# Kernel tuning notes

Measured on AMD Instinct MI355X. Metric: run time of the kernel, lower is better.

Reference implementation:

```python
import jax, jax.numpy as jnp
import numpy as np

B, L, H, NH, HD, M, NL, V, RD, NS = 4, 512, 768, 12, 64, 3072, 6, 32000, 128, 2
EPS = 1e-12
COEF = 1.0 / float(np.sqrt(HD))
NEG_INF = float('-inf')


def _ln(x, scale, bias):
    x = x - jnp.mean(x, axis=-1, keepdims=True)
    x = x * jax.lax.rsqrt(jnp.mean(jnp.square(x), axis=-1, keepdims=True) + EPS)
    return x * scale + bias


def setup_inputs() -> dict:
    key = jax.random.key(0)
    ks = jax.random.split(key, 16)
    def p(k, shape):
        return jax.random.normal(k, shape, jnp.float32) * 0.02
    return dict(
        token_ids=jax.random.randint(ks[0], (B, L), 0, V, jnp.int32),
        segment_ids=jax.random.randint(ks[1], (B, L), 0, NS, jnp.int32),
        input_mask=jnp.ones((B, L), jnp.int32),
        tok_emb=p(ks[2], (V, H)),
        seg_emb=p(ks[3], (NS, H)),
        emb_scale=jnp.ones((H,), jnp.float32),
        emb_bias=jnp.zeros((H,), jnp.float32),
        Wq=p(ks[4], (NL, H, NH, HD)), bq=jnp.zeros((NL, NH, HD), jnp.float32),
        Wk=p(ks[5], (NL, H, NH, HD)), bk=jnp.zeros((NL, NH, HD), jnp.float32),
        Wv=p(ks[6], (NL, H, NH, HD)), bv=jnp.zeros((NL, NH, HD), jnp.float32),
        relpos=p(ks[7], (NL, 2 * RD - 1, H)),
        Wo=p(ks[8], (NL, NH, HD, H)), bo=jnp.zeros((NL, H), jnp.float32),
        ln1_s=jnp.ones((NL, H), jnp.float32), ln1_b=jnp.zeros((NL, H), jnp.float32),
        W1=p(ks[9], (NL, H, M)), b1=jnp.zeros((NL, M), jnp.float32),
        W2=p(ks[10], (NL, M, H)), b2=jnp.zeros((NL, H), jnp.float32),
        ln2_s=jnp.ones((NL, H), jnp.float32), ln2_b=jnp.zeros((NL, H), jnp.float32),
    )


def _encoder(token_ids, segment_ids, input_mask,
             tok_emb, seg_emb, emb_scale, emb_bias,
             Wq, bq, Wk, bk, Wv, bv, relpos, Wo, bo,
             ln1_s, ln1_b, W1, b1, W2, b2, ln2_s, ln2_b):
    # Embedding block: token + segment embeddings, layer norm (dropout = eval/no-op)
    x = tok_emb[token_ids] + seg_emb[segment_ids]            # [B, L, H]
    x = _ln(x, emb_scale, emb_bias)
    mask = jnp.where(input_mask.astype(bool), 0.0, NEG_INF)[:, None, None, :]  # [B,1,1,L]

    for i in range(NL):
        # --- relative-position self-attention ---
        q = jnp.einsum('bqe,ehd->bqhd', x, Wq[i]) + bq[i]
        k = jnp.einsum('bke,ehd->bkhd', x, Wk[i]) + bk[i]
        v = jnp.einsum('bke,ehd->bkhd', x, Wv[i]) + bv[i]
        att = jnp.einsum('bqhd,bkhd->bhqk', q, k) + mask      # [B,NH,L,L]
        # skew trick: embed absolute [L,L] scores into relative [L, 2L-1] layout
        att = jnp.pad(att, [(0, 0), (0, 0), (0, 0), (0, L - 2)], constant_values=NEG_INF)
        att = att.reshape(att.shape[:2] + (L * (2 * L - 2),))
        att = jnp.pad(att, [(0, 0), (0, 0), (L - 1, 1)], constant_values=NEG_INF)
        att = att.reshape(att.shape[:2] + (L, 2 * L - 1))     # [B,NH,L,2L-1]
        # relative-position key/value embeddings, edge-padded to 2L-1 rows
        pad = L - RD
        rel_emb = jnp.pad(relpos[i], [(pad, pad), (0, 0)], mode='edge')  # [2L-1, H]
        k_rel = jnp.einsum('re,ehd->rhd', rel_emb, Wk[i]) + bk[i]
        att = (att + jnp.einsum('bqhd,rhd->bhqr', q, k_rel)) * COEF
        probs = jax.nn.softmax(att, axis=-1)                  # [B,NH,L,2L-1]
        v_rel = jnp.einsum('re,ehd->rhd', rel_emb, Wv[i]) + bv[i]
        rel_ctx = jnp.einsum('bhqr,rhd->bqhd', probs, v_rel)
        # un-skew probs back to [B,NH,L,L] for the absolute-position context
        p = probs.reshape(probs.shape[:2] + (L * (2 * L - 1),))[:, :, L - 1:-1]
        p = p.reshape(probs.shape[:2] + (L, 2 * L - 2))[:, :, :, :L]
        ctx = jnp.einsum('bhqk,bkhd->bqhd', p, v) + rel_ctx
        y = jnp.einsum('bqhd,hde->bqe', ctx, Wo[i]) + bo[i]
        x = _ln(x + y, ln1_s[i], ln1_b[i])
        # --- MLP block ---
        y = jax.nn.gelu(jnp.einsum('bqe,em->bqm', x, W1[i]) + b1[i])
        y = jnp.einsum('bqm,me->bqe', y, W2[i]) + b2[i]
        x = _ln(x + y, ln2_s[i], ln2_b[i])
    return x


def reference(token_ids, segment_ids, input_mask,
              tok_emb, seg_emb, emb_scale, emb_bias,
              Wq, bq, Wk, bk, Wv, bv, relpos, Wo, bo,
              ln1_s, ln1_b, W1, b1, W2, b2, ln2_s, ln2_b):
    return _encoder(token_ids, segment_ids, input_mask,
                    tok_emb, seg_emb, emb_scale, emb_bias,
                    Wq, bq, Wk, bk, Wv, bv, relpos, Wo, bo,
                    ln1_s, ln1_b, W1, b1, W2, b2, ln2_s, ln2_b)
```

## Files before the change

kernel.cpp:

```cpp
#include <hip/hip_runtime.h>
#include <hip/hip_bf16.h>
#include <math.h>

#define B_   4
#define L_   512
#define H_   768
#define NH_  12
#define HD_  64
#define M_   3072
#define NL_  6
#define RD_  128
#define NR_  255
#define ROWS (B_*L_)
#define MEXT 2304
#define COEF_ 0.125f

typedef __attribute__((ext_vector_type(8))) short bf16x8;
typedef __attribute__((ext_vector_type(4))) float f32x4;


static __device__ __forceinline__ float wave_reduce_sum(float v) {
#pragma unroll
    for (int off = 32; off > 0; off >>= 1) v += __shfl_xor(v, off, 64);
    return v;
}

static __device__ __forceinline__ float gelu_f(float x) {
    float x3 = x * x * x;
    return 0.5f * x * (1.f + tanhf(0.7978845608028654f * (x + 0.044715f * x3)));
}

static __device__ __forceinline__ unsigned short f2bfu(float v) {
    __hip_bfloat16 h = __float2bfloat16(v);
    return *(unsigned short*)&h;
}

static __device__ __forceinline__ float bfu2f(unsigned short u) {
    union { float f; unsigned int i; } x;
    x.i = ((unsigned int)u) << 16;
    return x.f;
}

static __device__ __forceinline__ void gload16(const void* g, void* l) {
    __builtin_amdgcn_global_load_lds(
        (const __attribute__((address_space(1))) void*)g,
        (__attribute__((address_space(3))) void*)l,
        16, 0, 0);
}


__global__ __launch_bounds__(256) void embed_ln_kernel(
    const int* __restrict__ tok, const int* __restrict__ seg,
    const float* __restrict__ temb, const float* __restrict__ semb,
    const float* __restrict__ sc, const float* __restrict__ bi,
    float* __restrict__ out, __hip_bfloat16* __restrict__ outb)
{
    int row = blockIdx.x;
    int t = threadIdx.x;
    int tid = tok[row], sid = seg[row];
    const float* tp = temb + (size_t)tid * H_;
    const float* sp = semb + (size_t)sid * H_;
    float v[3];
#pragma unroll
    for (int j = 0; j < 3; j++) { int idx = t + j * 256; v[j] = tp[idx] + sp[idx]; }

    __shared__ float red[4];
    __shared__ float bc;
    int lane = t & 63, wid = t >> 6;

    float s = v[0] + v[1] + v[2];
    s = wave_reduce_sum(s);
    if (lane == 0) red[wid] = s;
    __syncthreads();
    if (t == 0) bc = (red[0] + red[1] + red[2] + red[3]) * (1.f / H_);
    __syncthreads();
    float mean = bc;

    float c[3]; float ss = 0.f;
#pragma unroll
    for (int j = 0; j < 3; j++) { c[j] = v[j] - mean; ss += c[j] * c[j]; }
    ss = wave_reduce_sum(ss);
    __syncthreads();
    if (lane == 0) red[wid] = ss;
    __syncthreads();
    if (t == 0) bc = rsqrtf((red[0] + red[1] + red[2] + red[3]) * (1.f / H_) + 1e-12f);
    __syncthreads();
    float r = bc;
#pragma unroll
    for (int j = 0; j < 3; j++) {
        int idx = t + j * 256;
        float o = c[j] * r * sc[idx] + bi[idx];
        out[(size_t)row * H_ + idx] = o;
        outb[(size_t)row * H_ + idx] = __float2bfloat16(o);
    }
}


__global__ __launch_bounds__(256) void add_ln_kernel(
    const float* __restrict__ x, const float* __restrict__ p0,
    const float* __restrict__ p1, const float* __restrict__ p2,
    const float* __restrict__ bias,
    const float* __restrict__ sc, const float* __restrict__ bi,
    float* __restrict__ out, __hip_bfloat16* __restrict__ outb)
{
    int row = blockIdx.x;
    int t = threadIdx.x;
    const float* xp = x + (size_t)row * H_;
    const float* q0 = p0 + (size_t)row * H_;
    const float* q1 = p1 ? p1 + (size_t)row * H_ : nullptr;
    const float* q2 = p2 ? p2 + (size_t)row * H_ : nullptr;
    float v[3];
#pragma unroll
    for (int j = 0; j < 3; j++) {
        int idx = t + j * 256;
        float a = xp[idx] + q0[idx];
        if (q1) a += q1[idx];
        if (q2) a += q2[idx];
        if (bias) a += bias[idx];
        v[j] = a;
    }

    __shared__ float red[4];
    __shared__ float bc;
    int lane = t & 63, wid = t >> 6;

    float s = v[0] + v[1] + v[2];
    s = wave_reduce_sum(s);
    if (lane == 0) red[wid] = s;
    __syncthreads();
    if (t == 0) bc = (red[0] + red[1] + red[2] + red[3]) * (1.f / H_);
    __syncthreads();
    float mean = bc;

    float c[3]; float ss = 0.f;
#pragma unroll
    for (int j = 0; j < 3; j++) { c[j] = v[j] - mean; ss += c[j] * c[j]; }
    ss = wave_reduce_sum(ss);
    __syncthreads();
    if (lane == 0) red[wid] = ss;
    __syncthreads();
    if (t == 0) bc = rsqrtf((red[0] + red[1] + red[2] + red[3]) * (1.f / H_) + 1e-12f);
    __syncthreads();
    float r = bc;
#pragma unroll
    for (int j = 0; j < 3; j++) {
        int idx = t + j * 256;
        float o = c[j] * r * sc[idx] + bi[idx];
        out[(size_t)row * H_ + idx] = o;
        if (outb) outb[(size_t)row * H_ + idx] = __float2bfloat16(o);
    }
}


__global__ __launch_bounds__(256) void pack_all_kernel(
    const float* __restrict__ Wq, const float* __restrict__ Wk, const float* __restrict__ Wv,
    const float* __restrict__ Wo, const float* __restrict__ W1, const float* __restrict__ W2,
    const float* __restrict__ bq, const float* __restrict__ bk, const float* __restrict__ bv,
    const float* __restrict__ relpos,
    __hip_bfloat16* __restrict__ WtQ6, __hip_bfloat16* __restrict__ WtO6,
    __hip_bfloat16* __restrict__ WtW16, __hip_bfloat16* __restrict__ WtW26,
    float* __restrict__ qkvbias6, __hip_bfloat16* __restrict__ relb6)
{
    const int l = blockIdx.z / 7;
    const int zz = blockIdx.z % 7;
    const int t = threadIdx.x;
    if (zz == 6) {
        int id = blockIdx.y * 48 + blockIdx.x;
        if (id < 192) {
            int i = id * 1024 + t * 4;
            if (i < NR_ * H_) {
                float4 v = *(const float4*)(relpos + (size_t)l * NR_ * H_ + i);
                ushort4 o;
                o.x = f2bfu(v.x); o.y = f2bfu(v.y); o.z = f2bfu(v.z); o.w = f2bfu(v.w);
                *(ushort4*)((unsigned short*)relb6 + (size_t)l * NR_ * H_ + i) = o;
            }
        } else if (id < 201) {
            int i = (id - 192) * 256 + t;
            if (i < 2304) {
                float v = i < 768 ? bq[(size_t)l * H_ + i]
                        : (i < 1536 ? bk[(size_t)l * H_ + i - 768]
                                    : bv[(size_t)l * H_ + i - 1536]);
                qkvbias6[(size_t)l * 2304 + i] = v;
            }
        }
        return;
    }
    const float* in; __hip_bfloat16* out; int K, N;
    int bx = blockIdx.x, by = blockIdx.y;
    if (zz < 4) {
        if (bx >= 12) return;
        K = 768; N = 768;
        in = (zz == 0) ? Wq + (size_t)l * H_ * H_
           : (zz == 1) ? Wk + (size_t)l * H_ * H_
           : (zz == 2) ? Wv + (size_t)l * H_ * H_
                       : Wo + (size_t)l * H_ * H_;
        out = (zz < 3) ? WtQ6 + (size_t)l * 3 * H_ * H_ + (size_t)zz * H_ * H_
                       : WtO6 + (size_t)l * H_ * H_;
    } else if (zz == 4) {
        K = 768; N = 3072;
        in = W1 + (size_t)l * H_ * M_; out = WtW16 + (size_t)l * M_ * H_;
    } else {
        K = 3072; N = 768;
        in = W2 + (size_t)l * M_ * H_; out = WtW26 + (size_t)l * H_ * M_;
        int tmp = bx; bx = by; by = tmp;
    }
    __shared__ float tile[64][68];
    const int bX = bx * 64;
    const int bY = by * 64;
    {
        int r = t >> 2, c0 = (t & 3) * 16;
        const float* src = in + (size_t)(bY + r) * N + bX + c0;
#pragma unroll
        for (int i = 0; i < 4; i++)
            *(float4*)&tile[r][c0 + i * 4] = *(const float4*)(src + i * 4);
    }
    __syncthreads();
    {
        int n = t >> 2, k0 = (t & 3) * 16;
        unsigned short ov[16];
#pragma unroll
        for (int i = 0; i < 16; i++) ov[i] = f2bfu(tile[k0 + i][n]);
        unsigned short* dst = (unsigned short*)out + (size_t)(bX + n) * K + bY + k0;
        *(uint4*)dst       = *(uint4*)&ov[0];
        *(uint4*)(dst + 8) = *(uint4*)&ov[8];
    }
}


__global__ __launch_bounds__(256) void transpose_vvr_kernel(
    const __hip_bfloat16* __restrict__ qkvb,
    __hip_bfloat16* __restrict__ vT, __hip_bfloat16* __restrict__ vrT)
{
    __shared__ unsigned short tile[64][72];
    const int bx = blockIdx.x;
    const int h  = blockIdx.y;
    const int t = threadIdx.x;
    const int r = t >> 2, c0 = (t & 3) * 16;
    if (bx < 32) {
        const int kb = bx * 64;
        const unsigned short* src = (const unsigned short*)qkvb + (size_t)(kb + r) * 2304 + 1536 + h * 64 + c0;
        *(uint4*)&tile[r][c0]     = *(const uint4*)src;
        *(uint4*)&tile[r][c0 + 8] = *(const uint4*)(src + 8);
        __syncthreads();
        unsigned short outv[16];
#pragma unroll
        for (int i = 0; i < 16; i++) outv[i] = tile[c0 + i][r];
        unsigned short* dst = (unsigned short*)vT +
            ((size_t)((kb >> 9) * NH_ + h) * 64 + r) * 512 + (kb & 511) + c0;
        *(uint4*)dst       = *(uint4*)&outv[0];
        *(uint4*)(dst + 8) = *(uint4*)&outv[8];
    } else {
        const int jb = (bx - 32) * 64;
        const int j = jb + r;
        if (j < NR_) {
            const unsigned short* src = (const unsigned short*)qkvb + (size_t)(2048 + j) * 2304 + 1536 + h * 64 + c0;
            *(uint4*)&tile[r][c0]     = *(const uint4*)src;
            *(uint4*)&tile[r][c0 + 8] = *(const uint4*)(src + 8);
        } else {
#pragma unroll
            for (int i = 0; i < 16; i++) tile[r][c0 + i] = 0;
        }
        __syncthreads();
        unsigned short outv[16];
#pragma unroll
        for (int i = 0; i < 16; i++) outv[i] = tile[c0 + i][r];
        unsigned short* dst = (unsigned short*)vrT + ((size_t)(h * 64) + r) * 256 + jb + c0;
        *(uint4*)dst       = *(uint4*)&outv[0];
        *(uint4*)(dst + 8) = *(uint4*)&outv[8];
    }
}


#define TK 64

__global__ __launch_bounds__(512, 6) void gemm_bf16_kernel(
    const __hip_bfloat16* __restrict__ A, const __hip_bfloat16* __restrict__ A2,
    const __hip_bfloat16* __restrict__ Bt,
    const float* __restrict__ bias, float* __restrict__ Cf, __hip_bfloat16* __restrict__ Cb,
    float* __restrict__ CfX, size_t xstride,
    int M, int N, int K, int act, int ksplit)
{
    __shared__ __hip_bfloat16 As[2][128 * TK];
    __shared__ __hip_bfloat16 Bs[2][64 * TK];
    const int t = threadIdx.x;
    const int lane = t & 63;
    const int wid = t >> 6;
    const int lq = lane & 15, lg = lane >> 4;
    const int wm = (wid & 3) * 32, wn = (wid >> 2) * 32;

    const int nbx = gridDim.x;
    const int nwg = nbx * gridDim.y;
    int wgid = blockIdx.y * nbx + blockIdx.x;
    if ((nwg & 7) == 0) { int qq = nwg >> 3; wgid = (wgid & 7) * qq + (wgid >> 3); }
    const int bm = (wgid / nbx) * 128, bn = (wgid % nbx) * 64;
    const int kbase = blockIdx.z * ksplit;

    f32x4 acc[2][2];
#pragma unroll
    for (int i = 0; i < 2; i++)
#pragma unroll
        for (int j = 0; j < 2; j++) acc[i][j] = (f32x4){0.f, 0.f, 0.f, 0.f};

    const int rl = t >> 3;
    const int cswz = (((t & 7) * 16) ^ ((rl & 7) << 4)) >> 1;
    const __hip_bfloat16* ga[2];
    const __hip_bfloat16* gb;
    int lofsA[2], lofsB;
#pragma unroll
    for (int c = 0; c < 2; c++) {
        int rowa = bm + c * 64 + rl;
        const __hip_bfloat16* base;
        if (A2 && rowa >= ROWS) {
            int rr = rowa - ROWS; if (rr > NR_ - 1) rr = NR_ - 1;
            base = A2 + (size_t)rr * K;
        } else {
            if (rowa >= M) rowa = M - 1;
            base = A + (size_t)rowa * K;
        }
        ga[c] = base + kbase + cswz;
        lofsA[c] = (c * 64 + wid * 8) * TK;
    }
    gb = Bt + (size_t)(bn + rl) * K + kbase + cswz;
    lofsB = (wid * 8) * TK;

    const int nt = ksplit / TK;
    gload16(ga[0], &As[0][lofsA[0]]);
    gload16(ga[1], &As[0][lofsA[1]]);
    gload16(gb,    &Bs[0][lofsB]);
    __syncthreads();

    int cur = 0;
    for (int kt = 0; kt < nt; kt++) {
        if (kt + 1 < nt) {
            const int koff = (kt + 1) * TK;
            gload16(ga[0] + koff, &As[cur ^ 1][lofsA[0]]);
            gload16(ga[1] + koff, &As[cur ^ 1][lofsA[1]]);
            gload16(gb + koff,    &Bs[cur ^ 1][lofsB]);
        }
#pragma unroll
        for (int kh = 0; kh < 2; kh++) {
            const int kb = kh * 64 + lg * 16;
            bf16x8 af[2], bfr[2];
#pragma unroll
            for (int i = 0; i < 2; i++) {
                int ra = wm + i * 16 + lq;
                af[i] = *(const bf16x8*)((const char*)&As[cur][0] + ra * 128 + (kb ^ ((ra & 7) << 4)));
            }
#pragma unroll
            for (int j = 0; j < 2; j++) {
                int rb = wn + j * 16 + lq;
                bfr[j] = *(const bf16x8*)((const char*)&Bs[cur][0] + rb * 128 + (kb ^ ((rb & 7) << 4)));
            }
#pragma unroll
            for (int i = 0; i < 2; i++)
#pragma unroll
                for (int j = 0; j < 2; j++)
                    acc[i][j] = __builtin_amdgcn_mfma_f32_16x16x32_bf16(af[i], bfr[j], acc[i][j], 0, 0, 0);
        }
        __syncthreads();
        cur ^= 1;
    }

    float* outf = (blockIdx.z == 0) ? Cf : (CfX + (size_t)(blockIdx.z - 1) * xstride);
#pragma unroll
    for (int i = 0; i < 2; i++) {
#pragma unroll
        for (int j = 0; j < 2; j++) {
            int col = bn + wn + j * 16 + lq;
            float bsv = bias ? bias[col] : 0.f;
            int row0 = bm + wm + i * 16 + lg * 4;
#pragma unroll
            for (int rr = 0; rr < 4; rr++) {
                int row = row0 + rr;
                if (row >= M) continue;
                float v = acc[i][j][rr] + bsv;
                if (act) v = gelu_f(v);
                if (Cb && blockIdx.z == 0) Cb[(size_t)row * N + col] = __float2bfloat16(v);
                else                       outf[(size_t)row * N + col] = v;
            }
        }
    }
}


#define PS_LD 520
#define PR_LD 264

__global__ __launch_bounds__(256, 3) void attn_kernel(
    const __hip_bfloat16* __restrict__ qkvb,
    const __hip_bfloat16* __restrict__ vT,
    const __hip_bfloat16* __restrict__ vrT,
    const int* __restrict__ mask,
    __hip_bfloat16* __restrict__ ctxb)
{
    __shared__ unsigned short RqPrel[32 * PR_LD];
    __shared__ unsigned short Ps[32 * PS_LD];
    __shared__ float mstat[32 * 4];
    __shared__ float sstat[32 * 4];
    __shared__ float maskb[512];

    const int i_ = blockIdx.x;
    const int c_ = i_ & 7, s_ = i_ >> 3;
    const int p_ = c_ + 8 * (s_ >> 4);
    const int qt = s_ & 15;
    const int b = p_ / 12, h = p_ % 12;

    const int t = threadIdx.x;
    const int lane = t & 63, w = t >> 6;
    const int lq = lane & 15, lg = lane >> 4;

    maskb[t]       = mask[b * L_ + t]       ? 0.f : -1e30f;
    maskb[t + 256] = mask[b * L_ + t + 256] ? 0.f : -1e30f;

    const char* Qbase  = (const char*)qkvb + ((size_t)(b * L_ + qt * 32) * 2304 + h * 64) * 2;
    const char* Kbase  = (const char*)qkvb + ((size_t)(b * L_) * 2304 + 768 + h * 64) * 2;
    const char* KRbase = (const char*)qkvb + ((size_t)2048 * 2304 + 768 + h * 64) * 2;

    bf16x8 afq[2][2];
#pragma unroll
    for (int ks = 0; ks < 2; ks++) {
        const int kofs = ks * 64 + lg * 16;
        afq[ks][0] = *(const bf16x8*)(Qbase + (size_t)lq * 4608 + kofs);
        afq[ks][1] = *(const bf16x8*)(Qbase + (size_t)(16 + lq) * 4608 + kofs);
    }

    f32x4 accr[2][4];
#pragma unroll
    for (int i = 0; i < 2; i++)
#pragma unroll
        for (int j = 0; j < 4; j++) accr[i][j] = (f32x4){0.f, 0.f, 0.f, 0.f};
#pragma unroll
    for (int ks = 0; ks < 2; ks++) {
        const int kofs = ks * 64 + lg * 16;
        bf16x8 bkr_[4];
#pragma unroll
        for (int jt = 0; jt < 4; jt++) {
            int j = w * 64 + jt * 16 + lq;
            int jr = j > 254 ? 254 : j;
            bkr_[jt] = *(const bf16x8*)(KRbase + (size_t)jr * 4608 + kofs);
        }
#pragma unroll
        for (int jt = 0; jt < 4; jt++) {
            accr[0][jt] = __builtin_amdgcn_mfma_f32_16x16x32_bf16(afq[ks][0], bkr_[jt], accr[0][jt], 0, 0, 0);
            accr[1][jt] = __builtin_amdgcn_mfma_f32_16x16x32_bf16(afq[ks][1], bkr_[jt], accr[1][jt], 0, 0, 0);
        }
    }

    bf16x8 bk0_[8], bk1_[8];
#pragma unroll
    for (int jt = 0; jt < 8; jt++) {
        int key = w * 128 + jt * 16 + lq;
        bk0_[jt] = *(const bf16x8*)(Kbase + (size_t)key * 4608 + lg * 16);
        bk1_[jt] = *(const bf16x8*)(Kbase + (size_t)key * 4608 + 64 + lg * 16);
    }

#pragma unroll
    for (int it = 0; it < 2; it++)
#pragma unroll
        for (int jt = 0; jt < 4; jt++)
#pragma unroll
            for (int r = 0; r < 4; r++)
                RqPrel[(it * 16 + lg * 4 + r) * PR_LD + w * 64 + jt * 16 + lq] = f2bfu(accr[it][jt][r]);

    f32x4 accs[2][8];
#pragma unroll
    for (int i = 0; i < 2; i++)
#pragma unroll
        for (int j = 0; j < 8; j++) accs[i][j] = (f32x4){0.f, 0.f, 0.f, 0.f};
#pragma unroll
    for (int jt = 0; jt < 8; jt++) {
        accs[0][jt] = __builtin_amdgcn_mfma_f32_16x16x32_bf16(afq[0][0], bk0_[jt], accs[0][jt], 0, 0, 0);
        accs[1][jt] = __builtin_amdgcn_mfma_f32_16x16x32_bf16(afq[0][1], bk0_[jt], accs[1][jt], 0, 0, 0);
    }
#pragma unroll
    for (int jt = 0; jt < 8; jt++) {
        accs[0][jt] = __builtin_amdgcn_mfma_f32_16x16x32_bf16(afq[1][0], bk1_[jt], accs[0][jt], 0, 0, 0);
        accs[1][jt] = __builtin_amdgcn_mfma_f32_16x16x32_bf16(afq[1][1], bk1_[jt], accs[1][jt], 0, 0, 0);
    }

    const __hip_bfloat16* vTb  = vT  + (((size_t)(b * NH_ + h) * 64) + w * 16 + lq) * 512 + lg * 8;
    const __hip_bfloat16* vrTb = vrT + ((size_t)(h * 64) + w * 16 + lq) * 256 + lg * 8;
    bf16x8 vrpre[8];
#pragma unroll
    for (int ks = 0; ks < 8; ks++)
        vrpre[ks] = *(const bf16x8*)(vrTb + ks * 32);

    __syncthreads();

#pragma unroll
    for (int it = 0; it < 2; it++) {
#pragma unroll
        for (int r = 0; r < 4; r++) {
            int q = it * 16 + lg * 4 + r;
            int qg = qt * 32 + q;
            float mx = -INFINITY;
#pragma unroll
            for (int jt = 0; jt < 8; jt++) {
                int k = w * 128 + jt * 16 + lq;
                int jc = k - qg + 127;
                jc = jc < 0 ? 0 : (jc > 254 ? 254 : jc);
                float s = (accs[it][jt][r] + bfu2f(RqPrel[q * PR_LD + jc])) * COEF_ + maskb[k];
                accs[it][jt][r] = s;
                mx = fmaxf(mx, s);
            }
#pragma unroll
            for (int off = 1; off < 16; off <<= 1) mx = fmaxf(mx, __shfl_xor(mx, off, 64));
            if (lq == 0) mstat[q * 4 + w] = mx;
        }
    }
    __syncthreads();

#pragma unroll
    for (int it = 0; it < 2; it++) {
#pragma unroll
        for (int r = 0; r < 4; r++) {
            int q = it * 16 + lg * 4 + r;
            float4 mv = *(const float4*)&mstat[q * 4];
            float gm = fmaxf(fmaxf(mv.x, mv.y), fmaxf(mv.z, mv.w));
            float ssum = 0.f;
#pragma unroll
            for (int jt = 0; jt < 8; jt++) {
                int k = w * 128 + jt * 16 + lq;
                float p = __expf(accs[it][jt][r] - gm);
                ssum += p;
                Ps[q * PS_LD + k] = f2bfu(p);
            }
#pragma unroll
            for (int off = 1; off < 16; off <<= 1) ssum += __shfl_xor(ssum, off, 64);
            if (lq == 0) sstat[q * 4 + w] = ssum;
        }
    }
    __syncthreads();

    bf16x8 bvpre[8];
#pragma unroll
    for (int ks = 0; ks < 8; ks++)
        bvpre[ks] = *(const bf16x8*)(vTb + ks * 32);
    {
        int q = t >> 3, sub = t & 7;
        int qg = qt * 32 + q;
#pragma unroll
        for (int jj = 0; jj < 32; jj++) {
            int j = sub + 8 * jj;
            if (j == 0 || j == 254) continue;
            if (j == 255) { RqPrel[q * PR_LD + 255] = 0; continue; }
            int k = qg + j - 127;
            unsigned short val = ((unsigned)k < 512u) ? Ps[q * PS_LD + k] : (unsigned short)0;
            RqPrel[q * PR_LD + j] = val;
        }
    }
    {
        int task = t >> 2, ts = t & 3;
        int q = task >> 1, side = task & 1;
        int qg = qt * 32 + q;
        float sum = 0.f;
        if (side == 0) {
            int hi = qg - 127;
            for (int k = ts; k <= hi; k += 4) sum += bfu2f(Ps[q * PS_LD + k]);
        } else {
            for (int k = qg + 127 + ts; k < 512; k += 4) sum += bfu2f(Ps[q * PS_LD + k]);
        }
        sum += __shfl_xor(sum, 1, 64);
        sum += __shfl_xor(sum, 2, 64);
        if (ts == 0) RqPrel[q * PR_LD + (side == 0 ? 0 : 254)] = f2bfu(sum);
    }
    __syncthreads();

    f32x4 accv[2];
    accv[0] = (f32x4){0.f, 0.f, 0.f, 0.f};
    accv[1] = (f32x4){0.f, 0.f, 0.f, 0.f};

#pragma unroll
    for (int ks = 0; ks < 8; ks++) {
        bf16x8 pa0 = *(const bf16x8*)((const char*)Ps + (size_t)lq * (PS_LD * 2) + ks * 64 + lg * 16);
        bf16x8 pa1 = *(const bf16x8*)((const char*)Ps + (size_t)(16 + lq) * (PS_LD * 2) + ks * 64 + lg * 16);
        accv[0] = __builtin_amdgcn_mfma_f32_16x16x32_bf16(pa0, bvpre[ks], accv[0], 0, 0, 0);
        accv[1] = __builtin_amdgcn_mfma_f32_16x16x32_bf16(pa1, bvpre[ks], accv[1], 0, 0, 0);
    }
#pragma unroll
    for (int ks = 8; ks < 16; ks++) {
        bf16x8 bv = *(const bf16x8*)(vTb + ks * 32);
        bf16x8 pa0 = *(const bf16x8*)((const char*)Ps + (size_t)lq * (PS_LD * 2) + ks * 64 + lg * 16);
        bf16x8 pa1 = *(const bf16x8*)((const char*)Ps + (size_t)(16 + lq) * (PS_LD * 2) + ks * 64 + lg * 16);
        accv[0] = __builtin_amdgcn_mfma_f32_16x16x32_bf16(pa0, bv, accv[0], 0, 0, 0);
        accv[1] = __builtin_amdgcn_mfma_f32_16x16x32_bf16(pa1, bv, accv[1], 0, 0, 0);
    }
#pragma unroll
    for (int ks = 0; ks < 8; ks++) {
        bf16x8 pa0 = *(const bf16x8*)((const char*)RqPrel + (size_t)lq * (PR_LD * 2) + ks * 64 + lg * 16);
        bf16x8 pa1 = *(const bf16x8*)((const char*)RqPrel + (size_t)(16 + lq) * (PR_LD * 2) + ks * 64 + lg * 16);
        accv[0] = __builtin_amdgcn_mfma_f32_16x16x32_bf16(pa0, vrpre[ks], accv[0], 0, 0, 0);
        accv[1] = __builtin_amdgcn_mfma_f32_16x16x32_bf16(pa1, vrpre[ks], accv[1], 0, 0, 0);
    }

#pragma unroll
    for (int it = 0; it < 2; it++) {
#pragma unroll
        for (int r = 0; r < 4; r++) {
            int q = it * 16 + lg * 4 + r;
            float4 sv = *(const float4*)&sstat[q * 4];
            float inv = 1.f / (sv.x + sv.y + sv.z + sv.w);
            ctxb[(size_t)(b * L_ + qt * 32 + q) * 768 + h * 64 + w * 16 + lq] =
                __float2bfloat16(accv[it][r] * inv);
        }
    }
}


extern "C" void kernel_launch(void* const* d_in, const int* in_sizes, int n_in,
                              void* d_out, int out_size, void* d_ws, size_t ws_size,
                              hipStream_t stream)
{
    const int*   tok    = (const int*)d_in[0];
    const int*   seg    = (const int*)d_in[1];
    const int*   maskp  = (const int*)d_in[2];
    const float* temb   = (const float*)d_in[3];
    const float* semb   = (const float*)d_in[4];
    const float* esc    = (const float*)d_in[5];
    const float* ebi    = (const float*)d_in[6];
    const float* Wq     = (const float*)d_in[7];
    const float* bq     = (const float*)d_in[8];
    const float* Wk     = (const float*)d_in[9];
    const float* bk     = (const float*)d_in[10];
    const float* Wv     = (const float*)d_in[11];
    const float* bv     = (const float*)d_in[12];
    const float* relpos = (const float*)d_in[13];
    const float* Wo     = (const float*)d_in[14];
    const float* bo     = (const float*)d_in[15];
    const float* ln1s   = (const float*)d_in[16];
    const float* ln1b   = (const float*)d_in[17];
    const float* W1     = (const float*)d_in[18];
    const float* b1     = (const float*)d_in[19];
    const float* W2     = (const float*)d_in[20];
    const float* b2     = (const float*)d_in[21];
    const float* ln2s   = (const float*)d_in[22];
    const float* ln2b   = (const float*)d_in[23];

    const size_t NX = (size_t)ROWS * H_;
    float* x        = (float*)d_ws;
    float* x2       = x + NX;
    float* y        = x2 + NX;
    float* qkvbias6 = y + NX;
    __hip_bfloat16* xb    = (__hip_bfloat16*)(qkvbias6 + 6 * 2304);
    __hip_bfloat16* x2b   = xb    + NX;
    __hip_bfloat16* ctxb  = x2b   + NX;
    __hip_bfloat16* qkvb  = ctxb  + NX;
    __hip_bfloat16* vT    = qkvb  + (size_t)MEXT * 2304;
    __hip_bfloat16* vrT   = vT    + (size_t)B_ * NH_ * 64 * 512;
    __hip_bfloat16* relb6 = vrT   + (size_t)NH_ * 64 * 256;
    __hip_bfloat16* WtQ6  = relb6 + (size_t)NL_ * NR_ * H_;
    __hip_bfloat16* WtO6  = WtQ6  + (size_t)NL_ * 2304 * H_;
    __hip_bfloat16* WtW16 = WtO6  + (size_t)NL_ * H_ * H_;
    __hip_bfloat16* WtW26 = WtW16 + (size_t)NL_ * M_ * H_;
    __hip_bfloat16* h1b   = WtW26 + (size_t)NL_ * H_ * M_;

    float* spill = (float*)qkvb;

    dim3 blk(256);
    dim3 blk512(512);

    embed_ln_kernel<<<ROWS, blk, 0, stream>>>(tok, seg, temb, semb, esc, ebi, x, xb);
    pack_all_kernel<<<dim3(48, 12, NL_ * 7), blk, 0, stream>>>(
        Wq, Wk, Wv, Wo, W1, W2, bq, bk, bv, relpos,
        WtQ6, WtO6, WtW16, WtW26, qkvbias6, relb6);

    for (int l = 0; l < NL_; l++) {
        __hip_bfloat16* WtQ  = WtQ6  + (size_t)l * 2304 * H_;
        __hip_bfloat16* WtO  = WtO6  + (size_t)l * H_ * H_;
        __hip_bfloat16* WtW1 = WtW16 + (size_t)l * M_ * H_;
        __hip_bfloat16* WtW2 = WtW26 + (size_t)l * H_ * M_;
        __hip_bfloat16* relb = relb6 + (size_t)l * NR_ * H_;
        float* qkvbias = qkvbias6 + (size_t)l * 2304;

        gemm_bf16_kernel<<<dim3(36, 18), blk512, 0, stream>>>(xb, relb, WtQ, qkvbias,
                                                              nullptr, qkvb, nullptr, 0,
                                                              MEXT, 2304, H_, 0, H_);
        transpose_vvr_kernel<<<dim3(36, 12), blk, 0, stream>>>(qkvb, vT, vrT);

        attn_kernel<<<dim3(768), blk, 0, stream>>>(qkvb, vT, vrT, maskp, ctxb);

        gemm_bf16_kernel<<<dim3(12, 16, 2), blk512, 0, stream>>>(ctxb, nullptr, WtO, nullptr,
                                                                 y, nullptr, spill, NX,
                                                                 ROWS, H_, H_, 0, 384);
        add_ln_kernel<<<ROWS, blk, 0, stream>>>(x, y, spill, nullptr, bo + (size_t)l * H_,
                                                ln1s + (size_t)l * H_, ln1b + (size_t)l * H_, x2, x2b);

        gemm_bf16_kernel<<<dim3(48, 16), blk512, 0, stream>>>(x2b, nullptr, WtW1, b1 + (size_t)l * M_,
                                                              nullptr, h1b, nullptr, 0,
                                                              ROWS, M_, H_, 1, H_);
        gemm_bf16_kernel<<<dim3(12, 16, 3), blk512, 0, stream>>>(h1b, nullptr, WtW2, nullptr,
                                                                 y, nullptr, spill, NX,
                                                                 ROWS, H_, M_, 0, 1024);

        float* outp = (l == NL_ - 1) ? (float*)d_out : x;
        __hip_bfloat16* outbp = (l == NL_ - 1) ? nullptr : xb;
        add_ln_kernel<<<ROWS, blk, 0, stream>>>(x2, y, spill, spill + NX, b2 + (size_t)l * H_,
                                                ln2s + (size_t)l * H_, ln2b + (size_t)l * H_, outp, outbp);
    }
}
```

Measured before the change: 749.9 us.

## Restructure weight pack kernel into strip-based transpose with register prefetch

The weight transpose/convert kernel moves from a 3D grid with many early-exit blocks to a flat 1D grid. Each block now walks a 64-column strip over 12 k-tiles, double-buffering through shared memory with a register prefetch of the next tile. The aim is to remove idle blocks and overlap global loads with conversion and stores. The cost is fewer, longer-running blocks, and the store pattern changes to 8-byte writes.

```diff
diff --git a/kernel.cpp b/kernel.cpp
--- a/kernel.cpp
+++ b/kernel.cpp
@@ -161,22 +161,23 @@
     __hip_bfloat16* __restrict__ WtW16, __hip_bfloat16* __restrict__ WtW26,
     float* __restrict__ qkvbias6, __hip_bfloat16* __restrict__ relb6)
 {
-    const int l = blockIdx.z / 7;
-    const int zz = blockIdx.z % 7;
+    const int id = blockIdx.x;
     const int t = threadIdx.x;
-    if (zz == 6) {
-        int id = blockIdx.y * 48 + blockIdx.x;
-        if (id < 192) {
-            int i = id * 1024 + t * 4;
+
+    if (id >= 864) {
+        if (id < 2016) {
+            int rid = id - 864;
+            int l = rid / 192, seg = rid % 192;
+            int i = seg * 1024 + t * 4;
             if (i < NR_ * H_) {
                 float4 v = *(const float4*)(relpos + (size_t)l * NR_ * H_ + i);
                 ushort4 o;
                 o.x = f2bfu(v.x); o.y = f2bfu(v.y); o.z = f2bfu(v.z); o.w = f2bfu(v.w);
                 *(ushort4*)((unsigned short*)relb6 + (size_t)l * NR_ * H_ + i) = o;
             }
-        } else if (id < 201) {
-            int i = (id - 192) * 256 + t;
-            if (i < 2304) {
+        } else {
+            int l = id - 2016;
+            for (int i = t; i < 2304; i += 256) {
                 float v = i < 768 ? bq[(size_t)l * H_ + i]
                         : (i < 1536 ? bk[(size_t)l * H_ + i - 768]
                                     : bv[(size_t)l * H_ + i - 1536]);
@@ -185,44 +186,59 @@
         }
         return;
     }
-    const float* in; __hip_bfloat16* out; int K, N;
-    int bx = blockIdx.x, by = blockIdx.y;
-    if (zz < 4) {
-        if (bx >= 12) return;
-        K = 768; N = 768;
-        in = (zz == 0) ? Wq + (size_t)l * H_ * H_
-           : (zz == 1) ? Wk + (size_t)l * H_ * H_
-           : (zz == 2) ? Wv + (size_t)l * H_ * H_
-                       : Wo + (size_t)l * H_ * H_;
-        out = (zz < 3) ? WtQ6 + (size_t)l * 3 * H_ * H_ + (size_t)zz * H_ * H_
-                       : WtO6 + (size_t)l * H_ * H_;
-    } else if (zz == 4) {
-        K = 768; N = 3072;
+
+    const int l = id / 144;
+    const int r = id % 144;
+    const float* in; __hip_bfloat16* out; int K, N, strip, kb;
+    if (r < 48) {
+        int job = r / 12; strip = r % 12; K = 768; N = 768; kb = 0;
+        in = (job == 0) ? Wq + (size_t)l * H_ * H_
+           : (job == 1) ? Wk + (size_t)l * H_ * H_
+           : (job == 2) ? Wv + (size_t)l * H_ * H_
+                        : Wo + (size_t)l * H_ * H_;
+        out = (job < 3) ? WtQ6 + (size_t)l * 3 * H_ * H_ + (size_t)job * H_ * H_
+                        : WtO6 + (size_t)l * H_ * H_;
+    } else if (r < 96) {
+        strip = r - 48; K = 768; N = 3072; kb = 0;
         in = W1 + (size_t)l * H_ * M_; out = WtW16 + (size_t)l * M_ * H_;
     } else {
-        K = 3072; N = 768;
+        int q = r - 96; strip = q >> 2; kb = (q & 3) * 768; K = 3072; N = 768;
         in = W2 + (size_t)l * M_ * H_; out = WtW26 + (size_t)l * H_ * M_;
-        int tmp = bx; bx = by; by = tmp;
-    }
-    __shared__ float tile[64][68];
-    const int bX = bx * 64;
-    const int bY = by * 64;
+    }
+    const int bX = strip * 64;
+
+    __shared__ float tile[2][64][68];
+    const int kloc = t >> 2, c0 = (t & 3) * 16;
+    const int bi = t >> 4, bj = t & 15;
+
+    f32x4 rg[4];
     {
-        int r = t >> 2, c0 = (t & 3) * 16;
-        const float* src = in + (size_t)(bY + r) * N + bX + c0;
-#pragma unroll
-        for (int i = 0; i < 4; i++)
-            *(float4*)&tile[r][c0 + i * 4] = *(const float4*)(src + i * 4);
-    }
-    __syncthreads();
-    {
-        int n = t >> 2, k0 = (t & 3) * 16;
-        unsigned short ov[16];
-#pragma unroll
-        for (int i = 0; i < 16; i++) ov[i] = f2bfu(tile[k0 + i][n]);
-        unsigned short* dst = (unsigned short*)out + (size_t)(bX + n) * K + bY + k0;
-        *(uint4*)dst       = *(uint4*)&ov[0];
-        *(uint4*)(dst + 8) = *(uint4*)&ov[8];
+        const float* src = in + (size_t)(kb + kloc) * N + bX + c0;
+#pragma unroll
+        for (int i = 0; i < 4; i++) rg[i] = *(const f32x4*)(src + i * 4);
+    }
+
+    int cur = 0;
+    for (int kt = 0; kt < 12; kt++) {
+#pragma unroll
+        for (int i = 0; i < 4; i++) *(f32x4*)&tile[cur][kloc][c0 + i * 4] = rg[i];
+        if (kt + 1 < 12) {
+            const float* src = in + (size_t)(kb + (kt + 1) * 64 + kloc) * N + bX + c0;
+#pragma unroll
+            for (int i = 0; i < 4; i++) rg[i] = *(const f32x4*)(src + i * 4);
+        }
+        __syncthreads();
+        f32x4 v[4];
+#pragma unroll
+        for (int i = 0; i < 4; i++) v[i] = *(const f32x4*)&tile[cur][bj * 4 + i][bi * 4];
+#pragma unroll
+        for (int rr = 0; rr < 4; rr++) {
+            ushort4 o;
+            o.x = f2bfu(v[0][rr]); o.y = f2bfu(v[1][rr]);
+            o.z = f2bfu(v[2][rr]); o.w = f2bfu(v[3][rr]);
+            *(ushort4*)((unsigned short*)out + (size_t)(bX + bi * 4 + rr) * K + kb + kt * 64 + bj * 4) = o;
+        }
+        cur ^= 1;
     }
 }
 
@@ -660,7 +676,7 @@
     dim3 blk512(512);
 
     embed_ln_kernel<<<ROWS, blk, 0, stream>>>(tok, seg, temb, semb, esc, ebi, x, xb);
-    pack_all_kernel<<<dim3(48, 12, NL_ * 7), blk, 0, stream>>>(
+    pack_all_kernel<<<dim3(2022), blk, 0, stream>>>(
         Wq, Wk, Wv, Wo, W1, W2, bq, bk, bv, relpos,
         WtQ6, WtO6, WtW16, WtW26, qkvbias6, relb6);
 
```

Result: no change. 754.2 us (+0.6%).
